# Optimization experiments

Measured on AMD Instinct MI355X. Metric: run time of the kernel, lower is better.

The kernel has to match this reference:

```python
import jax, jax.numpy as jnp
import numpy as np

B, S, D = 2, 2048, 2048
H, KV, HD = 16, 4, 128          # n_heads, n_kv_heads, head_dim = d_model // n_heads
R = H // KV                      # n_rep (GQA group size)
THETA = 500000.0


def _rotate_half(x):
    x1, x2 = jnp.split(x, 2, axis=-1)
    return jnp.concatenate([-x2, x1], axis=-1)


def _rope_cos_sin(position_ids):
    # inv_freq over even dims, outer with positions, duplicated (LLaMA-style)
    inv_freq = 1.0 / (THETA ** (jnp.arange(0, HD, 2, dtype=jnp.float32) / HD))
    freqs = position_ids.astype(jnp.float32)[..., None] * inv_freq  # (B, S, HD/2)
    emb = jnp.concatenate([freqs, freqs], axis=-1)                  # (B, S, HD)
    return jnp.cos(emb)[:, None], jnp.sin(emb)[:, None]             # (B, 1, S, HD)


def setup_inputs() -> dict:
    key = jax.random.key(0)
    ks = jax.random.split(key, 5)
    x = jax.random.normal(ks[0], (B, S, D), dtype=jnp.float32)
    wq = jax.random.normal(ks[1], (D, H * HD), dtype=jnp.float32) * (D ** -0.5)
    wk = jax.random.normal(ks[2], (D, KV * HD), dtype=jnp.float32) * (D ** -0.5)
    wv = jax.random.normal(ks[3], (D, KV * HD), dtype=jnp.float32) * (D ** -0.5)
    wo = jax.random.normal(ks[4], (H * HD, D), dtype=jnp.float32) * (D ** -0.5)
    causal = jnp.tril(jnp.ones((S, S), dtype=bool))
    attn_mask = jnp.where(causal, 0.0, -1e9).astype(jnp.float32)[None, None]  # (1,1,S,S)
    position_ids = jnp.tile(jnp.arange(S, dtype=jnp.int32)[None, :], (B, 1))
    return {"x": x, "wq": wq, "wk": wk, "wv": wv, "wo": wo,
            "attn_mask": attn_mask, "position_ids": position_ids}


def reference(x, wq, wk, wv, wo, attn_mask, position_ids):
    b, s, _ = x.shape
    # projections (bias-free Linear) + head split, (B, heads, S, HD)
    q = (x @ wq).reshape(b, s, H, HD).transpose(0, 2, 1, 3)
    k = (x @ wk).reshape(b, s, KV, HD).transpose(0, 2, 1, 3)
    v = (x @ wv).reshape(b, s, KV, HD).transpose(0, 2, 1, 3)
    cos, sin = _rope_cos_sin(position_ids)
    q = q * cos + _rotate_half(q) * sin
    k = k * cos + _rotate_half(k) * sin
    # GQA: group q heads (B, KV, R, S, HD); equivalent to repeat_interleave on K/V
    qg = q.reshape(b, KV, R, s, HD)
    scores = jnp.einsum('bgrsd,bgtd->bgrst', qg.astype(jnp.float32),
                        k.astype(jnp.float32)) / np.float32(np.sqrt(HD))
    scores = scores + attn_mask[:, :, None]          # (1,1,1,S,S) broadcast
    p = jax.nn.softmax(scores, axis=-1).astype(x.dtype)
    out = jnp.einsum('bgrst,bgtd->bgrsd', p, v)      # (B, KV, R, S, HD)
    out = out.reshape(b, H, s, HD).transpose(0, 2, 1, 3).reshape(b, s, H * HD)
    return out @ wo
```

## Files before the change

### kernel.cpp

```cpp
#include <hip/hip_runtime.h>
#include <hip/hip_bf16.h>
#include <math.h>

#define Bsz 2
#define Sq  2048
#define Dm  2048
#define Hn  16
#define KVn 4
#define HDn 128

typedef __attribute__((ext_vector_type(8))) short bf16x8;
typedef __attribute__((ext_vector_type(4))) float f32x4;

__device__ __forceinline__ short f2b(float f) {
    __hip_bfloat16 h = __float2bfloat16(f);
    return *reinterpret_cast<short*>(&h);
}

__global__ __launch_bounds__(256) void f2b_kernel(
    const float* __restrict__ X, short* __restrict__ Y, int n4)
{
    int i = blockIdx.x * 256 + threadIdx.x;
    if (i >= n4) return;
    float4 v = ((const float4*)X)[i];
    short4 o;
    o.x = f2b(v.x); o.y = f2b(v.y); o.z = f2b(v.z); o.w = f2b(v.w);
    ((short4*)Y)[i] = o;
}

__global__ __launch_bounds__(256) void wconvT_kernel(
    const float* __restrict__ W, short* __restrict__ Wt, int N, int rowOff)
{
    __shared__ float t[32][33];
    const int k0 = blockIdx.y * 32;
    const int n0 = blockIdx.x * 32;
    const int tx = threadIdx.x, ty = threadIdx.y;
#pragma unroll
    for (int r = 0; r < 4; ++r) {
        const int row = ty + 8 * r;
        t[row][tx] = W[(size_t)(k0 + row) * N + n0 + tx];
    }
    __syncthreads();
#pragma unroll
    for (int r = 0; r < 4; ++r) {
        const int row = ty + 8 * r;
        Wt[(size_t)(rowOff + n0 + row) * Dm + k0 + tx] = f2b(t[tx][row]);
    }
}

__global__ __launch_bounds__(256) void gemm_bt_kernel(
    const short* __restrict__ A, const short* __restrict__ Bt,
    float* __restrict__ C, int M, int N, int K)
{
    __shared__ __align__(16) short As[128 * 64];
    __shared__ __align__(16) short Bs[128 * 64];

    const int tid  = threadIdx.x;
    const int w    = tid >> 6;
    const int lane = tid & 63;
    const int m16  = lane & 15;
    const int g4   = lane >> 4;
    const int wm   = w >> 1, wn = w & 1;

    const int row0 = blockIdx.y * 128;
    const int col0 = blockIdx.x * 128;

    const short* Ab = A  + (size_t)row0 * K;
    const short* Bb = Bt + (size_t)col0 * K;

    const int trow = tid >> 3;
    const int soct = (tid & 7) ^ (trow & 7);

    f32x4 acc[4][4];
#pragma unroll
    for (int i = 0; i < 4; ++i)
#pragma unroll
        for (int j = 0; j < 4; ++j) acc[i][j] = (f32x4){0.f, 0.f, 0.f, 0.f};

    for (int k0 = 0; k0 < K; k0 += 64) {
#pragma unroll
        for (int r = 0; r < 4; ++r) {
            const short* gp = Ab + (size_t)(r * 32 + trow) * K + k0 + soct * 8;
            short* lp = &As[(size_t)(r * 256 + w * 64) * 8];
            __builtin_amdgcn_global_load_lds(
                (const __attribute__((address_space(1))) void*)gp,
                (__attribute__((address_space(3))) void*)lp, 16, 0, 0);
        }
#pragma unroll
        for (int r = 0; r < 4; ++r) {
            const short* gp = Bb + (size_t)(r * 32 + trow) * K + k0 + soct * 8;
            short* lp = &Bs[(size_t)(r * 256 + w * 64) * 8];
            __builtin_amdgcn_global_load_lds(
                (const __attribute__((address_space(1))) void*)gp,
                (__attribute__((address_space(3))) void*)lp, 16, 0, 0);
        }
        __syncthreads();

#pragma unroll
        for (int kc = 0; kc < 2; ++kc) {
            bf16x8 a[4], b[4];
            const int swz = (kc * 4 + g4) ^ (m16 & 7);
#pragma unroll
            for (int s = 0; s < 4; ++s) {
                const int rowA = wm * 64 + s * 16 + m16;
                a[s] = *(const bf16x8*)&As[rowA * 64 + swz * 8];
                const int rowB = wn * 64 + s * 16 + m16;
                b[s] = *(const bf16x8*)&Bs[rowB * 64 + swz * 8];
            }
#pragma unroll
            for (int i = 0; i < 4; ++i)
#pragma unroll
                for (int j = 0; j < 4; ++j)
                    acc[i][j] = __builtin_amdgcn_mfma_f32_16x16x32_bf16(
                        a[i], b[j], acc[i][j], 0, 0, 0);
        }
        __syncthreads();
    }

#pragma unroll
    for (int i = 0; i < 4; ++i) {
        const int mbase = row0 + wm * 64 + i * 16 + g4 * 4;
#pragma unroll
        for (int j = 0; j < 4; ++j) {
            const int n = col0 + wn * 64 + j * 16 + m16;
#pragma unroll
            for (int r = 0; r < 4; ++r)
                C[(size_t)(mbase + r) * N + n] = acc[i][j][r];
        }
    }
}

__global__ __launch_bounds__(256) void rope_conv_kernel(
    const float* __restrict__ C3, short* __restrict__ Y,
    const int* __restrict__ pos_ids, int NHx, int colOff, float scale, int total)
{
    int idx = blockIdx.x * blockDim.x + threadIdx.x;
    if (idx >= total) return;
    const int i = idx & 63;
    int rest = idx >> 6;
    const int s = rest % Sq; rest /= Sq;
    const int h = rest % NHx;
    const int b = rest / NHx;

    const int pos = pos_ids[b * Sq + s];
    const float e   = -(float)(2 * i) * (1.0f / (float)HDn);
    const float inv = powf(500000.0f, e);
    const float f   = (float)pos * inv;
    const float c   = cosf(f);
    const float sn  = sinf(f);

    const float* src = C3 + ((size_t)(b * Sq + s)) * 3072 + colOff + h * HDn;
    const float x1 = src[i];
    const float x2 = src[i + 64];
    const size_t dst = (((size_t)b * NHx + h) * Sq + s) * HDn;
    Y[dst + i]      = f2b((x1 * c - x2 * sn) * scale);
    Y[dst + i + 64] = f2b((x2 * c + x1 * sn) * scale);
}

__global__ __launch_bounds__(256) void vconv_kernel(
    const float* __restrict__ C3, short* __restrict__ Vt)
{
    __shared__ float t[32][33];
    const int bk = blockIdx.z;
    const int b  = bk >> 2, kv = bk & 3;
    const int s0 = blockIdx.x * 32;
    const int d0 = blockIdx.y * 32;
    const int tx = threadIdx.x, ty = threadIdx.y;

#pragma unroll
    for (int r = 0; r < 4; ++r) {
        const int row = ty + 8 * r;
        t[row][tx] = C3[((size_t)(b * Sq + s0 + row)) * 3072 + 2560 + kv * HDn + d0 + tx];
    }
    __syncthreads();
#pragma unroll
    for (int r = 0; r < 4; ++r) {
        const int row = ty + 8 * r;
        Vt[((size_t)bk * HDn + d0 + row) * Sq + s0 + tx] = f2b(t[tx][row]);
    }
}

__global__ __launch_bounds__(256, 2) void fattn_kernel(
    const short* __restrict__ Qb, const short* __restrict__ Kb,
    const short* __restrict__ Vtb, short* __restrict__ AOb)
{
    __shared__ __align__(16) short Ks[64 * 128];
    __shared__ __align__(16) short Vs[128 * 64];

    const int tid  = threadIdx.x;
    const int w    = tid >> 6;
    const int lane = tid & 63;
    const int m16  = lane & 15;
    const int g4   = lane >> 4;

    const int i    = blockIdx.x;
    const int half = i >> 8;
    const int k4   = i & 15;
    const int qt   = half ? k4 : 15 - k4;
    const int bh   = i >> 4;
    const int h    = bh & 15;
    const int b    = bh >> 4;
    const int kv   = h >> 2;
    const int q0   = qt << 7;
    const int qA   = q0 + w * 16;
    const int qB   = q0 + 64 + w * 16;

    bf16x8 qf[2][4];
#pragma unroll
    for (int j = 0; j < 2; ++j) {
        const short* qp = Qb + (((size_t)b * Hn + h) * Sq + (j ? qB : qA) + m16) * HDn + g4 * 8;
#pragma unroll
        for (int c = 0; c < 4; ++c) qf[j][c] = *(const bf16x8*)(qp + c * 32);
    }

    const short* kbase = Kb  + ((size_t)b * KVn + kv) * Sq * HDn;
    const short* vbase = Vtb + ((size_t)b * KVn + kv) * (size_t)HDn * Sq;

    const short* gpK[4];
    const short* gpV[4];
#pragma unroll
    for (int r = 0; r < 4; ++r) {
        const int ci = r * 256 + tid;
        const int R  = ci >> 4, o = ci & 15;
        const int hf = (R >> 5) & 1, Rl = R & 31;
        const int phys = hf * 32 + ((Rl >> 2) & 3) * 8 + ((Rl >> 4) & 1) * 4 + (Rl & 3);
        gpK[r] = kbase + (size_t)phys * HDn + (o ^ (R & 7)) * 8;
        const int d = ci >> 3, ov = ci & 7;
        gpV[r] = vbase + (size_t)d * Sq + (ov ^ (d & 7)) * 8;
    }

    f32x4 Ot[2][8];
#pragma unroll
    for (int j = 0; j < 2; ++j)
#pragma unroll
        for (int t = 0; t < 8; ++t) Ot[j][t] = (f32x4){0.f, 0.f, 0.f, 0.f};
    float mcur[2] = {-1e30f, -1e30f}, lcur[2] = {0.f, 0.f};

    const int nch = qt * 2 + 2;
    for (int ch = 0; ch < nch; ++ch) {
        const int kt = ch << 6;

#pragma unroll
        for (int r = 0; r < 4; ++r) {
            const short* gp = gpK[r] + (size_t)kt * HDn;
            short* lp = &Ks[(size_t)(r * 256 + w * 64) * 8];
            __builtin_amdgcn_global_load_lds(
                (const __attribute__((address_space(1))) void*)gp,
                (__attribute__((address_space(3))) void*)lp, 16, 0, 0);
        }
#pragma unroll
        for (int r = 0; r < 4; ++r) {
            const short* gp = gpV[r] + kt;
            short* lp = &Vs[(size_t)(r * 256 + w * 64) * 8];
            __builtin_amdgcn_global_load_lds(
                (const __attribute__((address_space(1))) void*)gp,
                (__attribute__((address_space(3))) void*)lp, 16, 0, 0);
        }
        __syncthreads();

        const bool last  = (ch == nch - 1);
        const bool diag0 = (ch == nch - 2);

        f32x4 sc0[4], sc1[4];
#pragma unroll
        for (int f = 0; f < 4; ++f) {
            f32x4 a0 = (f32x4){0.f, 0.f, 0.f, 0.f};
            f32x4 a1 = (f32x4){0.f, 0.f, 0.f, 0.f};
            const int krow = f * 16 + m16;
#pragma unroll
            for (int c = 0; c < 4; ++c) {
                bf16x8 kf = *(const bf16x8*)&Ks[krow * 128 + (((c * 4 + g4) ^ (m16 & 7)) * 8)];
                a0 = __builtin_amdgcn_mfma_f32_16x16x32_bf16(kf, qf[0][c], a0, 0, 0, 0);
                a1 = __builtin_amdgcn_mfma_f32_16x16x32_bf16(kf, qf[1][c], a1, 0, 0, 0);
            }
            sc0[f] = a0; sc1[f] = a1;
        }

        if (diag0) {
            const int qg = qA + m16;
#pragma unroll
            for (int f = 0; f < 4; ++f)
#pragma unroll
                for (int ii = 0; ii < 4; ++ii) {
                    const int kg = kt + (f >> 1) * 32 + g4 * 8 + (f & 1) * 4 + ii;
                    if (kg > qg) sc0[f][ii] = -1e30f;
                }
        }
        if (last) {
            const int qg = qB + m16;
#pragma unroll
            for (int f = 0; f < 4; ++f)
#pragma unroll
                for (int ii = 0; ii < 4; ++ii) {
                    const int kg = kt + (f >> 1) * 32 + g4 * 8 + (f & 1) * 4 + ii;
                    if (kg > qg) sc1[f][ii] = -1e30f;
                }
        }

        bf16x8 pf0[2], pf1[2];
        if (!last) {
            float mx = sc0[0][0];
#pragma unroll
            for (int f = 0; f < 4; ++f)
#pragma unroll
                for (int ii = 0; ii < 4; ++ii) mx = fmaxf(mx, sc0[f][ii]);
            mx = fmaxf(mx, __shfl_xor(mx, 16));
            mx = fmaxf(mx, __shfl_xor(mx, 32));
            const float nm = fmaxf(mcur[0], mx);
            const float alpha = exp2f(mcur[0] - nm);
            mcur[0] = nm;
            float ps = 0.f;
#pragma unroll
            for (int f = 0; f < 4; ++f)
#pragma unroll
                for (int ii = 0; ii < 4; ++ii) {
                    sc0[f][ii] = exp2f(sc0[f][ii] - nm);
                    ps += sc0[f][ii];
                }
            ps += __shfl_xor(ps, 16);
            ps += __shfl_xor(ps, 32);
            lcur[0] = lcur[0] * alpha + ps;
#pragma unroll
            for (int t = 0; t < 8; ++t)
#pragma unroll
                for (int ii = 0; ii < 4; ++ii) Ot[0][t][ii] *= alpha;
#pragma unroll
            for (int hf = 0; hf < 2; ++hf) {
                bf16x8 p;
#pragma unroll
                for (int j8 = 0; j8 < 8; ++j8)
                    p[j8] = f2b(j8 < 4 ? sc0[hf * 2][j8] : sc0[hf * 2 + 1][j8 - 4]);
                pf0[hf] = p;
            }
        }
        {
            float mx = sc1[0][0];
#pragma unroll
            for (int f = 0; f < 4; ++f)
#pragma unroll
                for (int ii = 0; ii < 4; ++ii) mx = fmaxf(mx, sc1[f][ii]);
            mx = fmaxf(mx, __shfl_xor(mx, 16));
            mx = fmaxf(mx, __shfl_xor(mx, 32));
            const float nm = fmaxf(mcur[1], mx);
            const float alpha = exp2f(mcur[1] - nm);
            mcur[1] = nm;
            float ps = 0.f;
#pragma unroll
            for (int f = 0; f < 4; ++f)
#pragma unroll
                for (int ii = 0; ii < 4; ++ii) {
                    sc1[f][ii] = exp2f(sc1[f][ii] - nm);
                    ps += sc1[f][ii];
                }
            ps += __shfl_xor(ps, 16);
            ps += __shfl_xor(ps, 32);
            lcur[1] = lcur[1] * alpha + ps;
#pragma unroll
            for (int t = 0; t < 8; ++t)
#pragma unroll
                for (int ii = 0; ii < 4; ++ii) Ot[1][t][ii] *= alpha;
#pragma unroll
            for (int hf = 0; hf < 2; ++hf) {
                bf16x8 p;
#pragma unroll
                for (int j8 = 0; j8 < 8; ++j8)
                    p[j8] = f2b(j8 < 4 ? sc1[hf * 2][j8] : sc1[hf * 2 + 1][j8 - 4]);
                pf1[hf] = p;
            }
        }

#pragma unroll
        for (int t = 0; t < 8; ++t) {
            const int d = t * 16 + m16;
            bf16x8 vfa = *(const bf16x8*)&Vs[d * 64 + ((g4 ^ (d & 7)) * 8)];
            bf16x8 vfb = *(const bf16x8*)&Vs[d * 64 + (((4 + g4) ^ (d & 7)) * 8)];
            if (!last) {
                Ot[0][t] = __builtin_amdgcn_mfma_f32_16x16x32_bf16(vfa, pf0[0], Ot[0][t], 0, 0, 0);
                Ot[0][t] = __builtin_amdgcn_mfma_f32_16x16x32_bf16(vfb, pf0[1], Ot[0][t], 0, 0, 0);
            }
            Ot[1][t] = __builtin_amdgcn_mfma_f32_16x16x32_bf16(vfa, pf1[0], Ot[1][t], 0, 0, 0);
            Ot[1][t] = __builtin_amdgcn_mfma_f32_16x16x32_bf16(vfb, pf1[1], Ot[1][t], 0, 0, 0);
        }
        __syncthreads();
    }

#pragma unroll
    for (int j = 0; j < 2; ++j) {
        const float inv = 1.0f / lcur[j];
        short* op = AOb + ((size_t)b * Sq + (j ? qB : qA) + m16) * (Hn * HDn) + h * HDn + g4 * 4;
#pragma unroll
        for (int t = 0; t < 8; ++t) {
            short4 o;
            o.x = f2b(Ot[j][t][0] * inv);
            o.y = f2b(Ot[j][t][1] * inv);
            o.z = f2b(Ot[j][t][2] * inv);
            o.w = f2b(Ot[j][t][3] * inv);
            *(short4*)(op + t * 16) = o;
        }
    }
}

extern "C" void kernel_launch(void* const* d_in, const int* in_sizes, int n_in,
                              void* d_out, int out_size, void* d_ws, size_t ws_size,
                              hipStream_t stream)
{
    const float* x   = (const float*)d_in[0];
    const float* wq  = (const float*)d_in[1];
    const float* wk  = (const float*)d_in[2];
    const float* wv  = (const float*)d_in[3];
    const float* wo  = (const float*)d_in[4];
    const int* pos   = (const int*)d_in[6];
    float* out = (float*)d_out;

    const int M = Bsz * Sq;
    const size_t nX  = (size_t)M * Dm;

    short* xb    = (short*)d_ws;
    short* wqkvT = xb + nX;
    short* woT   = wqkvT + (size_t)3072 * Dm;
    float* C3    = (float*)(woT + (size_t)Dm * Dm);
    short* Qb    = (short*)(C3 + (size_t)M * 3072);
    short* Kb    = Qb + nX;
    short* Vtb   = Kb + (size_t)Bsz * KVn * Sq * HDn;
    short* AOb   = Vtb + (size_t)Bsz * KVn * Sq * HDn;

    f2b_kernel<<<(nX / 4 + 255) / 256, 256, 0, stream>>>(x, xb, nX / 4);
    {
        dim3 blk(32, 8);
        wconvT_kernel<<<dim3(2048 / 32, Dm / 32), blk, 0, stream>>>(wq, wqkvT, 2048, 0);
        wconvT_kernel<<<dim3(512 / 32,  Dm / 32), blk, 0, stream>>>(wk, wqkvT, 512,  2048);
        wconvT_kernel<<<dim3(512 / 32,  Dm / 32), blk, 0, stream>>>(wv, wqkvT, 512,  2560);
        wconvT_kernel<<<dim3(2048 / 32, Dm / 32), blk, 0, stream>>>(wo, woT,   2048, 0);
    }

    gemm_bt_kernel<<<dim3(3072 / 128, M / 128), 256, 0, stream>>>(
        xb, wqkvT, C3, M, 3072, Dm);

    {
        const float qscale = 0.08838834764831845f * 1.4426950408889634f;
        int totQ = Bsz * Hn * Sq * 64;
        rope_conv_kernel<<<(totQ + 255) / 256, 256, 0, stream>>>(
            C3, Qb, pos, Hn, 0, qscale, totQ);
        int totK = Bsz * KVn * Sq * 64;
        rope_conv_kernel<<<(totK + 255) / 256, 256, 0, stream>>>(
            C3, Kb, pos, KVn, 2048, 1.0f, totK);
    }
    vconv_kernel<<<dim3(Sq / 32, HDn / 32, Bsz * KVn), dim3(32, 8), 0, stream>>>(
        C3, Vtb);

    fattn_kernel<<<Bsz * Hn * (Sq / 128), 256, 0, stream>>>(Qb, Kb, Vtb, AOb);

    gemm_bt_kernel<<<dim3(Dm / 128, M / 128), 256, 0, stream>>>(
        AOb, woT, out, M, Dm, Dm);
}
```

Measured before the change: 376.7 us.

## Double-buffer attention K/V tiles, store QKV projection in bf16, merge conversion kernels

The attention kernel now keeps two LDS buffers for K and V. It issues the next chunk's async global-to-LDS loads right after the barrier, so the copy overlaps compute, and drops the trailing barrier. The QKV GEMM writes bf16 instead of fp32, halving the intermediate traffic read by the RoPE and V-transpose kernels. The four weight-transpose launches and the two RoPE launches are each merged into one kernel to reduce launch overhead. The risks are doubled LDS use in attention, which may limit occupancy at 2 blocks per CU, and an extra bf16 rounding of Q/K/V before RoPE.

```diff
diff --git a/kernel.cpp b/kernel.cpp
--- a/kernel.cpp
+++ b/kernel.cpp
@@ -16,6 +16,10 @@
     __hip_bfloat16 h = __float2bfloat16(f);
     return *reinterpret_cast<short*>(&h);
 }
+__device__ __forceinline__ float b2f(short s) {
+    __hip_bfloat16 h = *reinterpret_cast<__hip_bfloat16*>(&s);
+    return __bfloat162float(h);
+}
 
 __global__ __launch_bounds__(256) void f2b_kernel(
     const float* __restrict__ X, short* __restrict__ Y, int n4)
@@ -28,29 +32,39 @@
     ((short4*)Y)[i] = o;
 }
 
-__global__ __launch_bounds__(256) void wconvT_kernel(
-    const float* __restrict__ W, short* __restrict__ Wt, int N, int rowOff)
+__global__ __launch_bounds__(256) void wconv_all_kernel(
+    const float* __restrict__ wq, const float* __restrict__ wk,
+    const float* __restrict__ wv, const float* __restrict__ wo,
+    short* __restrict__ wqkvT, short* __restrict__ woT)
 {
     __shared__ float t[32][33];
+    const int n0 = blockIdx.x * 32;
     const int k0 = blockIdx.y * 32;
-    const int n0 = blockIdx.x * 32;
     const int tx = threadIdx.x, ty = threadIdx.y;
+
+    const float* W; int Nsec, nloc; short* dst;
+    if (n0 < 2048)      { W = wq; Nsec = 2048; nloc = n0;        dst = wqkvT + (size_t)n0 * Dm; }
+    else if (n0 < 2560) { W = wk; Nsec = 512;  nloc = n0 - 2048; dst = wqkvT + (size_t)n0 * Dm; }
+    else if (n0 < 3072) { W = wv; Nsec = 512;  nloc = n0 - 2560; dst = wqkvT + (size_t)n0 * Dm; }
+    else                { W = wo; Nsec = 2048; nloc = n0 - 3072; dst = woT + (size_t)(n0 - 3072) * Dm; }
+
 #pragma unroll
     for (int r = 0; r < 4; ++r) {
         const int row = ty + 8 * r;
-        t[row][tx] = W[(size_t)(k0 + row) * N + n0 + tx];
+        t[row][tx] = W[(size_t)(k0 + row) * Nsec + nloc + tx];
     }
     __syncthreads();
 #pragma unroll
     for (int r = 0; r < 4; ++r) {
         const int row = ty + 8 * r;
-        Wt[(size_t)(rowOff + n0 + row) * Dm + k0 + tx] = f2b(t[tx][row]);
-    }
-}
-
+        dst[(size_t)row * Dm + k0 + tx] = f2b(t[tx][row]);
+    }
+}
+
+template <typename OT>
 __global__ __launch_bounds__(256) void gemm_bt_kernel(
     const short* __restrict__ A, const short* __restrict__ Bt,
-    float* __restrict__ C, int M, int N, int K)
+    OT* __restrict__ C, int M, int N, int K)
 {
     __shared__ __align__(16) short As[128 * 64];
     __shared__ __align__(16) short Bs[128 * 64];
@@ -124,23 +138,34 @@
         for (int j = 0; j < 4; ++j) {
             const int n = col0 + wn * 64 + j * 16 + m16;
 #pragma unroll
-            for (int r = 0; r < 4; ++r)
-                C[(size_t)(mbase + r) * N + n] = acc[i][j][r];
-        }
-    }
-}
-
-__global__ __launch_bounds__(256) void rope_conv_kernel(
-    const float* __restrict__ C3, short* __restrict__ Y,
-    const int* __restrict__ pos_ids, int NHx, int colOff, float scale, int total)
+            for (int r = 0; r < 4; ++r) {
+                if constexpr (sizeof(OT) == 2)
+                    C[(size_t)(mbase + r) * N + n] = f2b(acc[i][j][r]);
+                else
+                    C[(size_t)(mbase + r) * N + n] = acc[i][j][r];
+            }
+        }
+    }
+}
+
+__global__ __launch_bounds__(256) void rope_all_kernel(
+    const short* __restrict__ C3b, short* __restrict__ Qb, short* __restrict__ Kb,
+    const int* __restrict__ pos_ids, float qscale, int total)
 {
     int idx = blockIdx.x * blockDim.x + threadIdx.x;
     if (idx >= total) return;
     const int i = idx & 63;
     int rest = idx >> 6;
-    const int s = rest % Sq; rest /= Sq;
-    const int h = rest % NHx;
-    const int b = rest / NHx;
+    const int s  = rest % Sq; rest /= Sq;
+    const int hh = rest % 20;
+    const int b  = rest / 20;
+
+    const bool isQ = hh < 16;
+    const int h      = isQ ? hh : hh - 16;
+    const int colOff = isQ ? 0 : 2048;
+    const int NHx    = isQ ? Hn : KVn;
+    const float scale = isQ ? qscale : 1.0f;
+    short* Y = isQ ? Qb : Kb;
 
     const int pos = pos_ids[b * Sq + s];
     const float e   = -(float)(2 * i) * (1.0f / (float)HDn);
@@ -149,18 +174,18 @@
     const float c   = cosf(f);
     const float sn  = sinf(f);
 
-    const float* src = C3 + ((size_t)(b * Sq + s)) * 3072 + colOff + h * HDn;
-    const float x1 = src[i];
-    const float x2 = src[i + 64];
+    const short* src = C3b + ((size_t)(b * Sq + s)) * 3072 + colOff + h * HDn;
+    const float x1 = b2f(src[i]);
+    const float x2 = b2f(src[i + 64]);
     const size_t dst = (((size_t)b * NHx + h) * Sq + s) * HDn;
     Y[dst + i]      = f2b((x1 * c - x2 * sn) * scale);
     Y[dst + i + 64] = f2b((x2 * c + x1 * sn) * scale);
 }
 
 __global__ __launch_bounds__(256) void vconv_kernel(
-    const float* __restrict__ C3, short* __restrict__ Vt)
-{
-    __shared__ float t[32][33];
+    const short* __restrict__ C3b, short* __restrict__ Vt)
+{
+    __shared__ short t[32][34];
     const int bk = blockIdx.z;
     const int b  = bk >> 2, kv = bk & 3;
     const int s0 = blockIdx.x * 32;
@@ -170,13 +195,13 @@
 #pragma unroll
     for (int r = 0; r < 4; ++r) {
         const int row = ty + 8 * r;
-        t[row][tx] = C3[((size_t)(b * Sq + s0 + row)) * 3072 + 2560 + kv * HDn + d0 + tx];
+        t[row][tx] = C3b[((size_t)(b * Sq + s0 + row)) * 3072 + 2560 + kv * HDn + d0 + tx];
     }
     __syncthreads();
 #pragma unroll
     for (int r = 0; r < 4; ++r) {
         const int row = ty + 8 * r;
-        Vt[((size_t)bk * HDn + d0 + row) * Sq + s0 + tx] = f2b(t[tx][row]);
+        Vt[((size_t)bk * HDn + d0 + row) * Sq + s0 + tx] = t[tx][row];
     }
 }
 
@@ -184,8 +209,8 @@
     const short* __restrict__ Qb, const short* __restrict__ Kb,
     const short* __restrict__ Vtb, short* __restrict__ AOb)
 {
-    __shared__ __align__(16) short Ks[64 * 128];
-    __shared__ __align__(16) short Vs[128 * 64];
+    __shared__ __align__(16) short Ks[2][64 * 128];
+    __shared__ __align__(16) short Vs[2][128 * 64];
 
     const int tid  = threadIdx.x;
     const int w    = tid >> 6;
@@ -237,13 +262,13 @@
     float mcur[2] = {-1e30f, -1e30f}, lcur[2] = {0.f, 0.f};
 
     const int nch = qt * 2 + 2;
-    for (int ch = 0; ch < nch; ++ch) {
-        const int kt = ch << 6;
-
+
+    auto stage = [&](int ch, int buf) {
+        const size_t kt = (size_t)(ch << 6);
 #pragma unroll
         for (int r = 0; r < 4; ++r) {
-            const short* gp = gpK[r] + (size_t)kt * HDn;
-            short* lp = &Ks[(size_t)(r * 256 + w * 64) * 8];
+            const short* gp = gpK[r] + kt * HDn;
+            short* lp = &Ks[buf][(size_t)(r * 256 + w * 64) * 8];
             __builtin_amdgcn_global_load_lds(
                 (const __attribute__((address_space(1))) void*)gp,
                 (__attribute__((address_space(3))) void*)lp, 16, 0, 0);
@@ -251,15 +276,27 @@
 #pragma unroll
         for (int r = 0; r < 4; ++r) {
             const short* gp = gpV[r] + kt;
-            short* lp = &Vs[(size_t)(r * 256 + w * 64) * 8];
+            short* lp = &Vs[buf][(size_t)(r * 256 + w * 64) * 8];
             __builtin_amdgcn_global_load_lds(
                 (const __attribute__((address_space(1))) void*)gp,
                 (__attribute__((address_space(3))) void*)lp, 16, 0, 0);
         }
+    };
+
+    stage(0, 0);
+
+    for (int ch = 0; ch < nch; ++ch) {
+        const int cur = ch & 1;
+        const int kt  = ch << 6;
+
         __syncthreads();
+        if (ch + 1 < nch) stage(ch + 1, cur ^ 1);
 
         const bool last  = (ch == nch - 1);
         const bool diag0 = (ch == nch - 2);
+
+        const short* KsC = Ks[cur];
+        const short* VsC = Vs[cur];
 
         f32x4 sc0[4], sc1[4];
 #pragma unroll
@@ -269,7 +306,7 @@
             const int krow = f * 16 + m16;
 #pragma unroll
             for (int c = 0; c < 4; ++c) {
-                bf16x8 kf = *(const bf16x8*)&Ks[krow * 128 + (((c * 4 + g4) ^ (m16 & 7)) * 8)];
+                bf16x8 kf = *(const bf16x8*)&KsC[krow * 128 + (((c * 4 + g4) ^ (m16 & 7)) * 8)];
                 a0 = __builtin_amdgcn_mfma_f32_16x16x32_bf16(kf, qf[0][c], a0, 0, 0, 0);
                 a1 = __builtin_amdgcn_mfma_f32_16x16x32_bf16(kf, qf[1][c], a1, 0, 0, 0);
             }
@@ -372,8 +409,8 @@
 #pragma unroll
         for (int t = 0; t < 8; ++t) {
             const int d = t * 16 + m16;
-            bf16x8 vfa = *(const bf16x8*)&Vs[d * 64 + ((g4 ^ (d & 7)) * 8)];
-            bf16x8 vfb = *(const bf16x8*)&Vs[d * 64 + (((4 + g4) ^ (d & 7)) * 8)];
+            bf16x8 vfa = *(const bf16x8*)&VsC[d * 64 + ((g4 ^ (d & 7)) * 8)];
+            bf16x8 vfb = *(const bf16x8*)&VsC[d * 64 + (((4 + g4) ^ (d & 7)) * 8)];
             if (!last) {
                 Ot[0][t] = __builtin_amdgcn_mfma_f32_16x16x32_bf16(vfa, pf0[0], Ot[0][t], 0, 0, 0);
                 Ot[0][t] = __builtin_amdgcn_mfma_f32_16x16x32_bf16(vfb, pf0[1], Ot[0][t], 0, 0, 0);
@@ -381,7 +418,6 @@
             Ot[1][t] = __builtin_amdgcn_mfma_f32_16x16x32_bf16(vfa, pf1[0], Ot[1][t], 0, 0, 0);
             Ot[1][t] = __builtin_amdgcn_mfma_f32_16x16x32_bf16(vfb, pf1[1], Ot[1][t], 0, 0, 0);
         }
-        __syncthreads();
     }
 
 #pragma unroll
@@ -418,38 +454,30 @@
     short* xb    = (short*)d_ws;
     short* wqkvT = xb + nX;
     short* woT   = wqkvT + (size_t)3072 * Dm;
-    float* C3    = (float*)(woT + (size_t)Dm * Dm);
-    short* Qb    = (short*)(C3 + (size_t)M * 3072);
+    short* C3b   = woT + (size_t)Dm * Dm;
+    short* Qb    = C3b + (size_t)M * 3072;
     short* Kb    = Qb + nX;
     short* Vtb   = Kb + (size_t)Bsz * KVn * Sq * HDn;
     short* AOb   = Vtb + (size_t)Bsz * KVn * Sq * HDn;
 
     f2b_kernel<<<(nX / 4 + 255) / 256, 256, 0, stream>>>(x, xb, nX / 4);
-    {
-        dim3 blk(32, 8);
-        wconvT_kernel<<<dim3(2048 / 32, Dm / 32), blk, 0, stream>>>(wq, wqkvT, 2048, 0);
-        wconvT_kernel<<<dim3(512 / 32,  Dm / 32), blk, 0, stream>>>(wk, wqkvT, 512,  2048);
-        wconvT_kernel<<<dim3(512 / 32,  Dm / 32), blk, 0, stream>>>(wv, wqkvT, 512,  2560);
-        wconvT_kernel<<<dim3(2048 / 32, Dm / 32), blk, 0, stream>>>(wo, woT,   2048, 0);
-    }
-
-    gemm_bt_kernel<<<dim3(3072 / 128, M / 128), 256, 0, stream>>>(
-        xb, wqkvT, C3, M, 3072, Dm);
+    wconv_all_kernel<<<dim3(5120 / 32, Dm / 32), dim3(32, 8), 0, stream>>>(
+        wq, wk, wv, wo, wqkvT, woT);
+
+    gemm_bt_kernel<short><<<dim3(3072 / 128, M / 128), 256, 0, stream>>>(
+        xb, wqkvT, C3b, M, 3072, Dm);
 
     {
         const float qscale = 0.08838834764831845f * 1.4426950408889634f;
-        int totQ = Bsz * Hn * Sq * 64;
-        rope_conv_kernel<<<(totQ + 255) / 256, 256, 0, stream>>>(
-            C3, Qb, pos, Hn, 0, qscale, totQ);
-        int totK = Bsz * KVn * Sq * 64;
-        rope_conv_kernel<<<(totK + 255) / 256, 256, 0, stream>>>(
-            C3, Kb, pos, KVn, 2048, 1.0f, totK);
+        int tot = Bsz * (Hn + KVn) * Sq * 64;
+        rope_all_kernel<<<(tot + 255) / 256, 256, 0, stream>>>(
+            C3b, Qb, Kb, pos, qscale, tot);
     }
     vconv_kernel<<<dim3(Sq / 32, HDn / 32, Bsz * KVn), dim3(32, 8), 0, stream>>>(
-        C3, Vtb);
+        C3b, Vtb);
 
     fattn_kernel<<<Bsz * Hn * (Sq / 128), 256, 0, stream>>>(Qb, Kb, Vtb, AOb);
 
-    gemm_bt_kernel<<<dim3(Dm / 128, M / 128), 256, 0, stream>>>(
+    gemm_bt_kernel<float><<<dim3(Dm / 128, M / 128), 256, 0, stream>>>(
         AOb, woT, out, M, Dm, Dm);
 }
```

New measurement: 348.7 us. 7.4% less time.
